# Performance work log

Hardware: AMD Instinct MI355X
Metric: run time of the kernel (lower is better)

Reference implementation:

```python
import jax, jax.numpy as jnp
import numpy as np

B, T, H = 32, 512, 1024
NT, NE = 8, 24          # padded per-sample trigger / entity span counts
C_TAGS = 50             # len(all_triggers_entities)
C = C_TAGS + 2          # + START/STOP for CRF
START, STOP = C_TAGS, C_TAGS + 1
A = 36                  # len(all_arguments)
D = 256                 # MLP hidden


def setup_inputs() -> dict:
    key = jax.random.key(0)
    ks = jax.random.split(key, 16)
    s = 0.02
    enc = jax.random.normal(ks[0], (B, T, H), jnp.float32)
    fc_W1 = jax.random.normal(ks[1], (H, D), jnp.float32) * s
    fc_b1 = jnp.zeros((D,), jnp.float32)
    fc_W2 = jax.random.normal(ks[2], (D, C), jnp.float32) * s
    fc_b2 = jnp.zeros((C,), jnp.float32)
    transitions = jax.random.normal(ks[3], (C, C), jnp.float32) * 0.01
    arg_W1 = jax.random.normal(ks[4], (2 * H, D), jnp.float32) * s
    arg_b1 = jnp.zeros((D,), jnp.float32)
    arg_W2 = jax.random.normal(ks[5], (D, A), jnp.float32) * s
    arg_b2 = jnp.zeros((A,), jnp.float32)
    tags = jax.random.randint(ks[6], (B, T), 0, C_TAGS)
    lengths = jax.random.randint(ks[7], (B,), T // 2, T + 1)
    trig_starts = jax.random.randint(ks[8], (B, NT), 0, T - 17)
    trig_ends = trig_starts + jax.random.randint(ks[9], (B, NT), 1, 17)
    trig_mask = (jnp.arange(NT)[None, :] < jax.random.randint(ks[10], (B, 1), 1, NT + 1)).astype(jnp.int32)
    ent_starts = jax.random.randint(ks[11], (B, NE), 0, T - 17)
    ent_ends = ent_starts + jax.random.randint(ks[12], (B, NE), 1, 17)
    ent_mask = (jnp.arange(NE)[None, :] < jax.random.randint(ks[13], (B, 1), 1, NE + 1)).astype(jnp.int32)
    return dict(encoder_out=enc, fc_W1=fc_W1, fc_b1=fc_b1, fc_W2=fc_W2, fc_b2=fc_b2,
                transitions=transitions, arg_W1=arg_W1, arg_b1=arg_b1, arg_W2=arg_W2, arg_b2=arg_b2,
                tags=tags, lengths=lengths,
                trig_starts=trig_starts, trig_ends=trig_ends, trig_mask=trig_mask,
                ent_starts=ent_starts, ent_ends=ent_ends, ent_mask=ent_mask)


def _crf_nll(feats, tags, mask, trans):
    # standard linear-chain CRF negative log likelihood, masked, summed over batch
    maskf = mask.astype(feats.dtype)
    alpha0 = feats[:, 0] + trans[START][None, :]            # [B,C]

    def step(alpha, xs):
        feat_t, m_t = xs                                    # [B,C], [B]
        new = jax.nn.logsumexp(alpha[:, :, None] + trans[None, :, :], axis=1) + feat_t
        return jnp.where(m_t[:, None] > 0, new, alpha), None

    alpha, _ = jax.lax.scan(step, alpha0,
                            (jnp.swapaxes(feats[:, 1:], 0, 1), jnp.swapaxes(mask[:, 1:], 0, 1)))
    logZ = jax.nn.logsumexp(alpha + trans[:, STOP][None, :], axis=1)  # [B]

    emit = jnp.take_along_axis(feats, tags[:, :, None], axis=2)[:, :, 0]
    emit_score = jnp.sum(emit * maskf, axis=1)
    trans_score = jnp.sum(trans[tags[:, :-1], tags[:, 1:]] * maskf[:, 1:], axis=1)
    start_score = trans[START, tags[:, 0]]
    last_idx = jnp.sum(mask, axis=1).astype(jnp.int32) - 1
    last_tag = jnp.take_along_axis(tags, last_idx[:, None], axis=1)[:, 0]
    stop_score = trans[last_tag, STOP]
    gold = emit_score + trans_score + start_score + stop_score
    return jnp.sum(logZ - gold)


def _span_mean(cs, starts, ends):
    # cs: exclusive prefix sums [B,T+1,H]; mean of encoder_out[i, s:e] per span
    s = jnp.take_along_axis(cs, starts[:, :, None], axis=1)
    e = jnp.take_along_axis(cs, ends[:, :, None], axis=1)
    return (e - s) / (ends - starts)[:, :, None].astype(cs.dtype)


def reference(encoder_out, fc_W1, fc_b1, fc_W2, fc_b2, transitions,
              arg_W1, arg_b1, arg_W2, arg_b2,
              tags, lengths, trig_starts, trig_ends, trig_mask,
              ent_starts, ent_ends, ent_mask):
    mask = (jnp.arange(T)[None, :] < lengths[:, None]).astype(jnp.int32)
    # trigger head: Linear -> Dropout(eval=identity) -> Linear (no activation, as in the source)
    feats = (encoder_out @ fc_W1 + fc_b1) @ fc_W2 + fc_b2   # [B,T,C]
    trigger_loss = _crf_nll(feats, tags, mask, transitions)

    # ragged span mean-pooling via prefix sums (replaces the per-sample python loop)
    cs = jnp.concatenate([jnp.zeros((B, 1, H), encoder_out.dtype),
                          jnp.cumsum(encoder_out, axis=1)], axis=1)  # [B,T+1,H]
    trig_vec = _span_mean(cs, trig_starts, trig_ends)       # [B,NT,H]
    ent_vec = _span_mean(cs, ent_starts, ent_ends)          # [B,NE,H]

    # cross product of (trigger, entity) per sample; concat order [entity, trigger]
    ent_b = jnp.broadcast_to(ent_vec[:, None, :, :], (B, NT, NE, H))
    trig_b = jnp.broadcast_to(trig_vec[:, :, None, :], (B, NT, NE, H))
    hidden = jnp.concatenate([ent_b, trig_b], axis=-1).reshape(B * NT * NE, 2 * H)
    logits = (hidden @ arg_W1 + arg_b1) @ arg_W2 + arg_b2   # [B*NT*NE, A]
    pair_mask = (trig_mask[:, :, None] * ent_mask[:, None, :]).reshape(-1).astype(logits.dtype)
    logits = logits * pair_mask[:, None]
    return trigger_loss, logits
```

## Files before the change

kernel.cpp:

```cpp
#include <hip/hip_runtime.h>
#include <math.h>

#define BB 32
#define TT 512
#define HH 1024
#define DD 256
#define CC 52
#define NTT 8
#define NEE 24
#define AA 36
#define STARTT 50
#define STOPP 51
#define NCH 16
#define CL 32

static const size_t OFF_WAT    = 0;
static const size_t OFF_BA     = 73728;
static const size_t OFF_ESTART = 73792;
static const size_t OFF_ESTOP  = 73856;
static const size_t OFF_BEFF   = 73920;
static const size_t OFF_EA     = 73984;
static const size_t OFF_WPACK  = 76032;
static const size_t OFF_FEATS  = 108800;
static const size_t OFF_EF64   = 960768;
static const size_t OFF_RMAT   = 2009344;
static const size_t OFF_TVEC   = 4106496;
static const size_t OFF_EVEC   = 4368640;
static const size_t OFF_TLOG   = 5155072;
static const size_t OFF_ELOG   = 5164288;
static const size_t OFF_LOSS   = 5191936;
static const size_t OFF_RED    = 5191968;

typedef __bf16 bf16x8 __attribute__((ext_vector_type(8)));
typedef float f32x4 __attribute__((ext_vector_type(4)));
typedef unsigned int uint4v __attribute__((ext_vector_type(4)));

union U4B { uint4v u; bf16x8 b; };

typedef const __attribute__((address_space(1))) void gvoid_t;
typedef __attribute__((address_space(3))) void lvoid_t;
#define GLOAD16(g, l) __builtin_amdgcn_global_load_lds((gvoid_t*)(g), (lvoid_t*)(l), 16, 0, 0)

static __device__ __forceinline__ unsigned int rne_bf16(float x) {
    unsigned int u = __float_as_uint(x);
    u += 0x7FFFu + ((u >> 16) & 1u);
    return u >> 16;
}

__global__ __launch_bounds__(256) void k1_prep_span(
    const float* __restrict__ enc,
    const float* __restrict__ fc_W1, const float* __restrict__ fc_b1,
    const float* __restrict__ fc_W2, const float* __restrict__ fc_b2,
    const float* __restrict__ trans,
    const float* __restrict__ arg_W1, const float* __restrict__ arg_b1,
    const float* __restrict__ arg_W2, const float* __restrict__ arg_b2,
    const int* __restrict__ ts, const int* __restrict__ te,
    const int* __restrict__ es, const int* __restrict__ ee,
    float* __restrict__ ws)
{
    int bid = blockIdx.x, tid = threadIdx.x;
    if (bid < 128) {
        int g = bid * 256 + tid;
        int s = g >> 2, i = g & 3;
        int kb = s >> 8, nb = (s >> 6) & 3, ln = s & 63;
        int c16 = ln & 15, hi = ln >> 4;
        int n = nb * 16 + c16;
        int k0 = kb * 32 + 8 * hi + 2 * i;
        unsigned int val = 0;
        if (n < CC) {
            const float* w1a = fc_W1 + (size_t)k0 * DD;
            const float* w1b = w1a + DD;
            float a0 = 0.f, a1 = 0.f;
            for (int d = 0; d < DD; ++d) {
                float w2 = fc_W2[d * CC + n];
                a0 = fmaf(w1a[d], w2, a0);
                a1 = fmaf(w1b[d], w2, a1);
            }
            val = rne_bf16(a0) | (rne_bf16(a1) << 16);
        }
        ((unsigned int*)(ws + OFF_WPACK))[g] = val;
    } else if (bid < 416) {
        int f = (bid - 128) * 256 + tid;
        int h = f / 36, a = f - h * 36;
        const float* w1 = arg_W1 + (size_t)h * DD;
        const float* w2 = arg_W2 + a;
        float a0 = 0.f, a1 = 0.f, a2 = 0.f, a3 = 0.f;
        for (int d = 0; d < DD; d += 4) {
            float4 w = *(const float4*)&w1[d];
            a0 = fmaf(w.x, w2[(size_t)(d + 0) * AA], a0);
            a1 = fmaf(w.y, w2[(size_t)(d + 1) * AA], a1);
            a2 = fmaf(w.z, w2[(size_t)(d + 2) * AA], a2);
            a3 = fmaf(w.w, w2[(size_t)(d + 3) * AA], a3);
        }
        ws[OFF_WAT + f] = (a0 + a1) + (a2 + a3);
    } else if (bid < 1440) {
        int sid = bid - 416;
        int b = sid >> 5, s = sid & 31;
        int st, en; float* outv;
        if (s < NTT) {
            st = ts[b * NTT + s]; en = te[b * NTT + s];
            outv = ws + OFF_TVEC + ((size_t)b * NTT + s) * HH;
        } else {
            int e = s - NTT;
            st = es[b * NEE + e]; en = ee[b * NEE + e];
            outv = ws + OFF_EVEC + ((size_t)b * NEE + e) * HH;
        }
        int h4 = tid * 4;
        float ax = 0, ay = 0, az = 0, aw = 0;
        for (int t = st; t < en; ++t) {
            float4 v = *(const float4*)&enc[((size_t)b * TT + t) * HH + h4];
            ax += v.x; ay += v.y; az += v.z; aw += v.w;
        }
        float inv = 1.f / (float)(en - st);
        float4 o; o.x = ax * inv; o.y = ay * inv; o.z = az * inv; o.w = aw * inv;
        *(float4*)&outv[h4] = o;
    } else {
        int f = (bid - 1440) * 256 + tid;
        if (f < 2048) {
            int m = f >> 5, kp = f & 31;
            int k0 = 2 * kp;
            unsigned int wlo = 0, whi = 0;
            if (m < 52) {
                if (k0 < 52)     wlo = rne_bf16(expf(trans[k0 * CC + m]) * 0.015625f);
                if (k0 + 1 < 52) whi = rne_bf16(expf(trans[(k0 + 1) * CC + m]) * 0.015625f);
            }
            ((unsigned int*)(ws + OFF_EA))[f] = wlo | (whi << 16);
        } else if (f < 2112) {
            int j = f - 2048;
            ws[OFF_ESTART + j] = (j < 52) ? expf(trans[STARTT * CC + j]) : 0.f;
        } else if (f < 2176) {
            int j = f - 2112;
            ws[OFF_ESTOP + j] = (j < 52) ? expf(trans[j * CC + STOPP]) : 0.f;
        } else if (f < 2240) {
            int c = f - 2176;
            float acc = 0.f;
            if (c < 52) {
                acc = fc_b2[c];
                for (int d = 0; d < DD; ++d) acc = fmaf(fc_b1[d], fc_W2[d * CC + c], acc);
            }
            ws[OFF_BEFF + c] = acc;
        } else if (f < 2304) {
            int a = f - 2240;
            float acc = 0.f;
            if (a < 36) {
                acc = arg_b2[a];
                for (int d = 0; d < DD; ++d) acc = fmaf(arg_b1[d], arg_W2[d * AA + a], acc);
            }
            ws[OFF_BA + a] = acc;
        } else if (f < 2306) {
            ((unsigned*)(ws + OFF_RED))[f - 2304] = 0u;
        }
    }
}

__global__ __launch_bounds__(256) void k2_feats_arg(
    const float* __restrict__ enc, float* __restrict__ ws)
{
    __shared__ f32x4 Ab[2][1024];
    __shared__ uint4v Bb[2][512];
    int bid = blockIdx.x, tid = threadIdx.x;
    int wid = tid >> 6, lane = tid & 63;

    if (bid >= 256) {
        int id = (bid - 256) * 4 + wid;
        int b = id >> 5, s = id & 31;
        int a = lane;
        const float* vec; const float* wt; float* outv; float base;
        if (s < NTT) {
            vec = ws + OFF_TVEC + ((size_t)b * NTT + s) * HH;
            wt  = ws + OFF_WAT + (size_t)1024 * AA;
            outv = ws + OFF_TLOG + ((size_t)b * NTT + s) * AA;
            base = (a < AA) ? ws[OFF_BA + a] : 0.f;
        } else {
            int e = s - NTT;
            vec = ws + OFF_EVEC + ((size_t)b * NEE + e) * HH;
            wt  = ws + OFF_WAT;
            outv = ws + OFF_ELOG + ((size_t)b * NEE + e) * AA;
            base = 0.f;
        }
        if (a < AA) {
            float a0 = 0, a1 = 0, a2 = 0, a3 = 0;
            for (int h = 0; h < HH; h += 4) {
                float4 vv = *(const float4*)&vec[h];
                a0 = fmaf(vv.x, wt[(size_t)(h + 0) * AA + a], a0);
                a1 = fmaf(vv.y, wt[(size_t)(h + 1) * AA + a], a1);
                a2 = fmaf(vv.z, wt[(size_t)(h + 2) * AA + a], a2);
                a3 = fmaf(vv.w, wt[(size_t)(h + 3) * AA + a], a3);
            }
            outv[a] = base + ((a0 + a1) + (a2 + a3));
        }
        return;
    }

    const uint4v* Wpack = (const uint4v*)(ws + OFF_WPACK);
    float* feats = ws + OFF_FEATS;
    float* ef64  = ws + OFF_EF64;
    int c16 = lane & 15, hi = lane >> 4;
    int c7 = c16 & 7;
    int row0 = bid * 64;
    int rowW = wid * 16 + c16;

    f32x4 acc[4];
#pragma unroll
    for (int nb = 0; nb < 4; ++nb) {
        float bv = ws[OFF_BEFF + nb * 16 + c16];
        acc[nb][0] = bv; acc[nb][1] = bv; acc[nb][2] = bv; acc[nb][3] = bv;
    }
    {
#pragma unroll
        for (int i = 0; i < 4; ++i) {
            int f = i * 256 + tid;
            int row = f >> 4, qp = f & 15;
            int q = (qp & 8) | ((qp & 7) ^ (row & 7));
            GLOAD16(enc + (size_t)(row0 + row) * HH + q * 4, &Ab[0][i * 256 + wid * 64]);
        }
#pragma unroll
        for (int i = 0; i < 2; ++i) {
            GLOAD16(Wpack + i * 256 + tid, &Bb[0][i * 256 + wid * 64]);
        }
    }
    for (int it = 0; it < 16; ++it) {
        __syncthreads();
        if (it < 15) {
            int buf = (it + 1) & 1;
            int k0 = (it + 1) * 64;
#pragma unroll
            for (int i = 0; i < 4; ++i) {
                int f = i * 256 + tid;
                int row = f >> 4, qp = f & 15;
                int q = (qp & 8) | ((qp & 7) ^ (row & 7));
                GLOAD16(enc + (size_t)(row0 + row) * HH + k0 + q * 4, &Ab[buf][i * 256 + wid * 64]);
            }
#pragma unroll
            for (int i = 0; i < 2; ++i) {
                GLOAD16(Wpack + (size_t)(it + 1) * 512 + i * 256 + tid, &Bb[buf][i * 256 + wid * 64]);
            }
        }
        int cb = it & 1;
#pragma unroll
        for (int kbL = 0; kbL < 2; ++kbL) {
            int q0 = (kbL * 8) | ((2 * hi) ^ c7);
            int q1 = q0 ^ 1;
            f32x4 a0 = Ab[cb][rowW * 16 + q0];
            f32x4 a1 = Ab[cb][rowW * 16 + q1];
            f32x4 lo = (c7 & 1) ? a1 : a0;
            f32x4 hf = (c7 & 1) ? a0 : a1;
            unsigned u0, u1, u2, u3;
            asm("v_cvt_pk_bf16_f32 %0, %1, %2" : "=v"(u0) : "v"(lo[0]), "v"(lo[1]));
            asm("v_cvt_pk_bf16_f32 %0, %1, %2" : "=v"(u1) : "v"(lo[2]), "v"(lo[3]));
            asm("v_cvt_pk_bf16_f32 %0, %1, %2" : "=v"(u2) : "v"(hf[0]), "v"(hf[1]));
            asm("v_cvt_pk_bf16_f32 %0, %1, %2" : "=v"(u3) : "v"(hf[2]), "v"(hf[3]));
            U4B A; A.u[0] = u0; A.u[1] = u1; A.u[2] = u2; A.u[3] = u3;
#pragma unroll
            for (int nb = 0; nb < 4; ++nb) {
                U4B Bf; Bf.u = Bb[cb][kbL * 256 + nb * 64 + lane];
                acc[nb] = __builtin_amdgcn_mfma_f32_16x16x32_bf16(A.b, Bf.b, acc[nb], 0, 0, 0);
            }
        }
    }
#pragma unroll
    for (int nb = 0; nb < 4; ++nb) {
        int col = nb * 16 + c16;
#pragma unroll
        for (int r = 0; r < 4; ++r) {
            size_t grow = row0 + wid * 16 + hi * 4 + r;
            float v = acc[nb][r];
            if (col < CC) {
                feats[grow * CC + col] = v;
                ef64[grow * 64 + col] = expf(v);
            } else {
                ef64[grow * 64 + col] = 0.f;
            }
        }
    }
}

__global__ __launch_bounds__(64) void k3_chunk(
    const int* __restrict__ lengths, float* __restrict__ ws)
{
    int bid = blockIdx.x;
    int lane = threadIdx.x;

    const unsigned short* EA = (const unsigned short*)(ws + OFF_EA);
    const float* ef64 = ws + OFF_EF64;
    unsigned int* Rout = (unsigned int*)(ws + OFF_RMAT);
    int b = bid >> 6;
    int ch = (bid >> 2) & (NCH - 1);
    int nb = bid & 3;
    int c16 = lane & 15, hi = lane >> 4;
    int len = lengths[b];
    int t0 = 1 + ch * CL;
    int Le = len - t0; if (Le > CL) Le = CL;
    unsigned int* outm = Rout + (((size_t)b * NCH + ch) << 11);

    if (Le <= 0) {
#pragma unroll
        for (int q = 0; q < 8; ++q) {
            int col0 = nb * 16 + 2 * q;
            unsigned int val = 0;
            if (lane < 52) {
                if (col0 == lane)          val = 0x3F80u;
                else if (col0 + 1 == lane) val = 0x3F800000u;
            }
            outm[lane * 32 + nb * 8 + q] = val;
        }
        return;
    }

    bf16x8 Afr[4][2];
#pragma unroll
    for (int mb = 0; mb < 4; ++mb)
#pragma unroll
        for (int kb = 0; kb < 2; ++kb) {
            U4B x; x.u = *(const uint4v*)(EA + (size_t)(mb * 16 + c16) * 64 + kb * 32 + 8 * hi);
            Afr[mb][kb] = x.b;
        }

    unsigned int Bw[2][4];
#pragma unroll
    for (int kb = 0; kb < 2; ++kb)
#pragma unroll
        for (int j = 0; j < 4; ++j) {
            int col = nb * 16 + c16;
            int k0 = kb * 32 + 8 * hi + 2 * j;
            unsigned int v = 0;
            if (col < 52) {
                if (k0 == col)          v = 0x3F80u;
                else if (k0 + 1 == col) v = 0x3F800000u;
            }
            Bw[kb][j] = v;
        }

    unsigned int W[4][2];
    int hsel = hi >> 1;
    int src0 = c16 + 32 * (hi & 1);
    int src1 = src0 + 16;
    const float* efb = ef64 + (size_t)b * TT * 64;

    for (int s = 0; s < Le; ++s) {
        int t = t0 + s;
        U4B b0; b0.u = uint4v{Bw[0][0], Bw[0][1], Bw[0][2], Bw[0][3]};
        U4B b1; b1.u = uint4v{Bw[1][0], Bw[1][1], Bw[1][2], Bw[1][3]};
        f32x4 D[4];
#pragma unroll
        for (int mb = 0; mb < 4; ++mb) {
            f32x4 z = {0.f, 0.f, 0.f, 0.f};
            z = __builtin_amdgcn_mfma_f32_16x16x32_bf16(Afr[mb][0], b0.b, z, 0, 0, 0);
            z = __builtin_amdgcn_mfma_f32_16x16x32_bf16(Afr[mb][1], b1.b, z, 0, 0, 0);
            D[mb] = z;
        }
#pragma unroll
        for (int mb = 0; mb < 4; ++mb) {
            f32x4 cv = *(const f32x4*)(efb + (size_t)t * 64 + mb * 16 + 4 * hi);
            float d0 = D[mb][0] * cv[0];
            float d1 = D[mb][1] * cv[1];
            float d2 = D[mb][2] * cv[2];
            float d3 = D[mb][3] * cv[3];
            unsigned int w0, w1;
            asm("v_cvt_pk_bf16_f32 %0, %1, %2" : "=v"(w0) : "v"(d0), "v"(d1));
            asm("v_cvt_pk_bf16_f32 %0, %1, %2" : "=v"(w1) : "v"(d2), "v"(d3));
            W[mb][0] = w0; W[mb][1] = w1;
        }
#pragma unroll
        for (int kb = 0; kb < 2; ++kb)
#pragma unroll
            for (int j = 0; j < 4; ++j) {
                int src = (j < 2) ? src0 : src1;
                unsigned int va = (unsigned int)__shfl((int)W[2 * kb][j & 1], src, 64);
                unsigned int vb = (unsigned int)__shfl((int)W[2 * kb + 1][j & 1], src, 64);
                Bw[kb][j] = hsel ? vb : va;
            }
    }

#pragma unroll
    for (int mb = 0; mb < 4; ++mb)
#pragma unroll
        for (int w = 0; w < 2; ++w) {
            unsigned int my = W[mb][w];
            unsigned int ot = (unsigned int)__shfl_xor((int)my, 1, 64);
            unsigned int val;
            int r = 16 * mb + 4 * hi + 2 * w + (c16 & 1);
            if ((c16 & 1) == 0) val = (my & 0xFFFFu) | (ot << 16);
            else                val = (ot >> 16) | (my & 0xFFFF0000u);
            outm[r * 32 + nb * 8 + (c16 >> 1)] = val;
        }
}

__global__ __launch_bounds__(256) void k4_final(
    const float* __restrict__ trans,
    const int* __restrict__ tags, const int* __restrict__ lengths,
    const int* __restrict__ tmask, const int* __restrict__ emask,
    float* __restrict__ ws, float* __restrict__ out)
{
    __shared__ float vsh[64];
    int bid = blockIdx.x, tid = threadIdx.x;
    if (bid >= 32) {
        int idx = (bid - 32) * 256 + tid;
        int a = idx % AA;
        int p = idx / AA;
        int ne = p % NEE;
        int q = p / NEE;
        int nt = q & 7;
        int b = q >> 3;
        float m = (float)(tmask[b * NTT + nt] * emask[b * NEE + ne]);
        out[1 + idx] = (ws[OFF_TLOG + ((size_t)b * NTT + nt) * AA + a] +
                        ws[OFF_ELOG + ((size_t)b * NEE + ne) * AA + a]) * m;
        return;
    }
    if (tid >= 64) return;
    int b = bid, lane = tid;
    int len = lengths[b];
    const unsigned int* Rb = (const unsigned int*)(ws + OFF_RMAT) + ((size_t)b << 15);
    float v = 0.f;
    if (lane < 52) v = ws[OFF_ESTART + lane] * ws[OFF_EF64 + (size_t)b * TT * 64 + lane];
    int S = 0;

    uint4v bf0[8], bf1[8], bf2[8];

#define LOADM(BUF, IDX)                                                        \
    {                                                                          \
        const unsigned int* rr = Rb + (size_t)(IDX) * 2048 + (size_t)lane * 32;\
        _Pragma("unroll")                                                      \
        for (int q = 0; q < 8; ++q) BUF[q] = *(const uint4v*)(rr + q * 4);     \
    }

#define MATVEC(BUF)                                                            \
    {                                                                          \
        vsh[lane] = v;                                                         \
        float c0 = 0, c1 = 0, c2 = 0, c3 = 0;                                  \
        _Pragma("unroll")                                                      \
        for (int q = 0; q < 8; ++q) {                                          \
            uint4v u = BUF[q];                                                 \
            float4 va = *(const float4*)&vsh[q * 8];                           \
            float4 vb = *(const float4*)&vsh[q * 8 + 4];                       \
            c0 = fmaf(__uint_as_float(u[0] << 16), va.x, c0);                  \
            c0 = fmaf(__uint_as_float(u[0] & 0xFFFF0000u), va.y, c0);          \
            c1 = fmaf(__uint_as_float(u[1] << 16), va.z, c1);                  \
            c1 = fmaf(__uint_as_float(u[1] & 0xFFFF0000u), va.w, c1);          \
            c2 = fmaf(__uint_as_float(u[2] << 16), vb.x, c2);                  \
            c2 = fmaf(__uint_as_float(u[2] & 0xFFFF0000u), vb.y, c2);          \
            c3 = fmaf(__uint_as_float(u[3] << 16), vb.z, c3);                  \
            c3 = fmaf(__uint_as_float(u[3] & 0xFFFF0000u), vb.w, c3);          \
        }                                                                      \
        float acc = (c0 + c1) + (c2 + c3);                                     \
        float M = acc;                                                         \
        _Pragma("unroll")                                                      \
        for (int o = 32; o >= 1; o >>= 1) M = fmaxf(M, __shfl_xor(M, o, 64));  \
        int e = (int)((__float_as_uint(M) >> 23) & 0xFF) - 127;                \
        acc *= __uint_as_float((unsigned)(127 - e) << 23);                     \
        S += e; v = acc;                                                       \
    }

    LOADM(bf0, 0) LOADM(bf1, 1)
    LOADM(bf2,  2) MATVEC(bf0)
    LOADM(bf0,  3) MATVEC(bf1)
    LOADM(bf1,  4) MATVEC(bf2)
    LOADM(bf2,  5) MATVEC(bf0)
    LOADM(bf0,  6) MATVEC(bf1)
    LOADM(bf1,  7) MATVEC(bf2)
    LOADM(bf2,  8) MATVEC(bf0)
    LOADM(bf0,  9) MATVEC(bf1)
    LOADM(bf1, 10) MATVEC(bf2)
    LOADM(bf2, 11) MATVEC(bf0)
    LOADM(bf0, 12) MATVEC(bf1)
    LOADM(bf1, 13) MATVEC(bf2)
    LOADM(bf2, 14) MATVEC(bf0)
    LOADM(bf0, 15) MATVEC(bf1)
    MATVEC(bf2)
    MATVEC(bf0)
#undef LOADM
#undef MATVEC

    float z = (lane < 52) ? v * ws[OFF_ESTOP + lane] : 0.f;
#pragma unroll
    for (int o = 32; o >= 1; o >>= 1) z += __shfl_xor(z, o, 64);
    float logZ = logf(z) + (float)(S + 6 * (len - 1)) * 0.6931471805599453f;

    const int* tg = tags + (size_t)b * TT;
    const float* fb = ws + OFF_FEATS + (size_t)b * TT * CC;
    float g = 0.f;
    for (int t = lane; t < TT; t += 64) {
        if (t < len) {
            int ct = tg[t];
            g += fb[(size_t)t * CC + ct];
            if (t + 1 < len) g += trans[ct * CC + tg[t + 1]];
        }
    }
#pragma unroll
    for (int o = 32; o >= 1; o >>= 1) g += __shfl_xor(g, o, 64);

    unsigned old = 0;
    if (lane == 0) {
        g += trans[STARTT * CC + tg[0]] + trans[tg[len - 1] * CC + STOPP];
        ws[OFF_LOSS + b] = logZ - g;
        __threadfence();
        unsigned* lcnt = (unsigned*)(ws + OFF_RED);
        old = __hip_atomic_fetch_add(lcnt, 1u, __ATOMIC_ACQ_REL, __HIP_MEMORY_SCOPE_AGENT);
    }
    old = (unsigned)__shfl((int)old, 0, 64);
    if (old == BB - 1) {
        __threadfence();
        float tv = (lane < BB) ? ((volatile float*)(ws + OFF_LOSS))[lane] : 0.f;
#pragma unroll
        for (int o = 32; o >= 1; o >>= 1) tv += __shfl_xor(tv, o, 64);
        if (lane == 0) out[0] = tv;
    }
}

extern "C" void kernel_launch(void* const* d_in, const int* in_sizes, int n_in,
                              void* d_out, int out_size, void* d_ws, size_t ws_size,
                              hipStream_t stream)
{
    const float* enc    = (const float*)d_in[0];
    const float* fc_W1  = (const float*)d_in[1];
    const float* fc_b1  = (const float*)d_in[2];
    const float* fc_W2  = (const float*)d_in[3];
    const float* fc_b2  = (const float*)d_in[4];
    const float* trans  = (const float*)d_in[5];
    const float* arg_W1 = (const float*)d_in[6];
    const float* arg_b1 = (const float*)d_in[7];
    const float* arg_W2 = (const float*)d_in[8];
    const float* arg_b2 = (const float*)d_in[9];
    const int* tags     = (const int*)d_in[10];
    const int* lengths  = (const int*)d_in[11];
    const int* tstarts  = (const int*)d_in[12];
    const int* tends    = (const int*)d_in[13];
    const int* tmask    = (const int*)d_in[14];
    const int* estarts  = (const int*)d_in[15];
    const int* eends    = (const int*)d_in[16];
    const int* emask    = (const int*)d_in[17];
    float* out = (float*)d_out;
    float* ws  = (float*)d_ws;

    hipLaunchKernelGGL(k1_prep_span, dim3(1450), dim3(256), 0, stream,
                       enc, fc_W1, fc_b1, fc_W2, fc_b2, trans,
                       arg_W1, arg_b1, arg_W2, arg_b2,
                       tstarts, tends, estarts, eends, ws);
    hipLaunchKernelGGL(k2_feats_arg, dim3(512), dim3(256), 0, stream,
                       enc, ws);
    hipLaunchKernelGGL(k3_chunk, dim3(2048), dim3(64), 0, stream,
                       lengths, ws);
    hipLaunchKernelGGL(k4_final, dim3(896), dim3(256), 0, stream,
                       trans, tags, lengths, tmask, emask, ws, out);
}
```

Baseline: 102.9 us.

## Move arg-logit blocks into chunk kernel, pack chunk waves, deepen matrix prefetch

The per-span argument-logit matvec blocks move out of the feats GEMM kernel and into the CRF chunk kernel, so the GEMM launches only its 256 MFMA tiles. The chunk kernel now packs four 64-lane chunk tasks per 256-thread block (512 blocks) and appends the arg-logit blocks after them, for 768 blocks in total. Separately, the final CRF chain matvec now cycles through four register buffers instead of three, keeping more matrix loads in flight at the cost of extra registers. The aim is to balance load across kernels, cut block count, and hide more global-load latency in the serial chain, with some risk to occupancy.

Result: faster. 100.0 us (-2.8%).

```diff
diff --git a/kernel.cpp b/kernel.cpp
--- a/kernel.cpp
+++ b/kernel.cpp
@@ -153,7 +153,7 @@
     }
 }
 
-__global__ __launch_bounds__(256) void k2_feats_arg(
+__global__ __launch_bounds__(256) void k2_feats(
     const float* __restrict__ enc, float* __restrict__ ws)
 {
     __shared__ f32x4 Ab[2][1024];
@@ -161,8 +161,97 @@
     int bid = blockIdx.x, tid = threadIdx.x;
     int wid = tid >> 6, lane = tid & 63;
 
-    if (bid >= 256) {
-        int id = (bid - 256) * 4 + wid;
+    const uint4v* Wpack = (const uint4v*)(ws + OFF_WPACK);
+    float* feats = ws + OFF_FEATS;
+    float* ef64  = ws + OFF_EF64;
+    int c16 = lane & 15, hi = lane >> 4;
+    int c7 = c16 & 7;
+    int row0 = bid * 64;
+    int rowW = wid * 16 + c16;
+
+    f32x4 acc[4];
+#pragma unroll
+    for (int nb = 0; nb < 4; ++nb) {
+        float bv = ws[OFF_BEFF + nb * 16 + c16];
+        acc[nb][0] = bv; acc[nb][1] = bv; acc[nb][2] = bv; acc[nb][3] = bv;
+    }
+    {
+#pragma unroll
+        for (int i = 0; i < 4; ++i) {
+            int f = i * 256 + tid;
+            int row = f >> 4, qp = f & 15;
+            int q = (qp & 8) | ((qp & 7) ^ (row & 7));
+            GLOAD16(enc + (size_t)(row0 + row) * HH + q * 4, &Ab[0][i * 256 + wid * 64]);
+        }
+#pragma unroll
+        for (int i = 0; i < 2; ++i) {
+            GLOAD16(Wpack + i * 256 + tid, &Bb[0][i * 256 + wid * 64]);
+        }
+    }
+    for (int it = 0; it < 16; ++it) {
+        __syncthreads();
+        if (it < 15) {
+            int buf = (it + 1) & 1;
+            int k0 = (it + 1) * 64;
+#pragma unroll
+            for (int i = 0; i < 4; ++i) {
+                int f = i * 256 + tid;
+                int row = f >> 4, qp = f & 15;
+                int q = (qp & 8) | ((qp & 7) ^ (row & 7));
+                GLOAD16(enc + (size_t)(row0 + row) * HH + k0 + q * 4, &Ab[buf][i * 256 + wid * 64]);
+            }
+#pragma unroll
+            for (int i = 0; i < 2; ++i) {
+                GLOAD16(Wpack + (size_t)(it + 1) * 512 + i * 256 + tid, &Bb[buf][i * 256 + wid * 64]);
+            }
+        }
+        int cb = it & 1;
+#pragma unroll
+        for (int kbL = 0; kbL < 2; ++kbL) {
+            int q0 = (kbL * 8) | ((2 * hi) ^ c7);
+            int q1 = q0 ^ 1;
+            f32x4 a0 = Ab[cb][rowW * 16 + q0];
+            f32x4 a1 = Ab[cb][rowW * 16 + q1];
+            f32x4 lo = (c7 & 1) ? a1 : a0;
+            f32x4 hf = (c7 & 1) ? a0 : a1;
+            unsigned u0, u1, u2, u3;
+            asm("v_cvt_pk_bf16_f32 %0, %1, %2" : "=v"(u0) : "v"(lo[0]), "v"(lo[1]));
+            asm("v_cvt_pk_bf16_f32 %0, %1, %2" : "=v"(u1) : "v"(lo[2]), "v"(lo[3]));
+            asm("v_cvt_pk_bf16_f32 %0, %1, %2" : "=v"(u2) : "v"(hf[0]), "v"(hf[1]));
+            asm("v_cvt_pk_bf16_f32 %0, %1, %2" : "=v"(u3) : "v"(hf[2]), "v"(hf[3]));
+            U4B A; A.u[0] = u0; A.u[1] = u1; A.u[2] = u2; A.u[3] = u3;
+#pragma unroll
+            for (int nb = 0; nb < 4; ++nb) {
+                U4B Bf; Bf.u = Bb[cb][kbL * 256 + nb * 64 + lane];
+                acc[nb] = __builtin_amdgcn_mfma_f32_16x16x32_bf16(A.b, Bf.b, acc[nb], 0, 0, 0);
+            }
+        }
+    }
+#pragma unroll
+    for (int nb = 0; nb < 4; ++nb) {
+        int col = nb * 16 + c16;
+#pragma unroll
+        for (int r = 0; r < 4; ++r) {
+            size_t grow = row0 + wid * 16 + hi * 4 + r;
+            float v = acc[nb][r];
+            if (col < CC) {
+                feats[grow * CC + col] = v;
+                ef64[grow * 64 + col] = expf(v);
+            } else {
+                ef64[grow * 64 + col] = 0.f;
+            }
+        }
+    }
+}
+
+__global__ __launch_bounds__(256) void k3_chunk_arg(
+    const int* __restrict__ lengths, float* __restrict__ ws)
+{
+    int bid = blockIdx.x, tid = threadIdx.x;
+    int wid = tid >> 6, lane = tid & 63;
+
+    if (bid >= 512) {
+        int id = (bid - 512) * 4 + wid;
         int b = id >> 5, s = id & 31;
         int a = lane;
         const float* vec; const float* wt; float* outv; float base;
@@ -192,101 +281,13 @@
         return;
     }
 
-    const uint4v* Wpack = (const uint4v*)(ws + OFF_WPACK);
-    float* feats = ws + OFF_FEATS;
-    float* ef64  = ws + OFF_EF64;
-    int c16 = lane & 15, hi = lane >> 4;
-    int c7 = c16 & 7;
-    int row0 = bid * 64;
-    int rowW = wid * 16 + c16;
-
-    f32x4 acc[4];
-#pragma unroll
-    for (int nb = 0; nb < 4; ++nb) {
-        float bv = ws[OFF_BEFF + nb * 16 + c16];
-        acc[nb][0] = bv; acc[nb][1] = bv; acc[nb][2] = bv; acc[nb][3] = bv;
-    }
-    {
-#pragma unroll
-        for (int i = 0; i < 4; ++i) {
-            int f = i * 256 + tid;
-            int row = f >> 4, qp = f & 15;
-            int q = (qp & 8) | ((qp & 7) ^ (row & 7));
-            GLOAD16(enc + (size_t)(row0 + row) * HH + q * 4, &Ab[0][i * 256 + wid * 64]);
-        }
-#pragma unroll
-        for (int i = 0; i < 2; ++i) {
-            GLOAD16(Wpack + i * 256 + tid, &Bb[0][i * 256 + wid * 64]);
-        }
-    }
-    for (int it = 0; it < 16; ++it) {
-        __syncthreads();
-        if (it < 15) {
-            int buf = (it + 1) & 1;
-            int k0 = (it + 1) * 64;
-#pragma unroll
-            for (int i = 0; i < 4; ++i) {
-                int f = i * 256 + tid;
-                int row = f >> 4, qp = f & 15;
-                int q = (qp & 8) | ((qp & 7) ^ (row & 7));
-                GLOAD16(enc + (size_t)(row0 + row) * HH + k0 + q * 4, &Ab[buf][i * 256 + wid * 64]);
-            }
-#pragma unroll
-            for (int i = 0; i < 2; ++i) {
-                GLOAD16(Wpack + (size_t)(it + 1) * 512 + i * 256 + tid, &Bb[buf][i * 256 + wid * 64]);
-            }
-        }
-        int cb = it & 1;
-#pragma unroll
-        for (int kbL = 0; kbL < 2; ++kbL) {
-            int q0 = (kbL * 8) | ((2 * hi) ^ c7);
-            int q1 = q0 ^ 1;
-            f32x4 a0 = Ab[cb][rowW * 16 + q0];
-            f32x4 a1 = Ab[cb][rowW * 16 + q1];
-            f32x4 lo = (c7 & 1) ? a1 : a0;
-            f32x4 hf = (c7 & 1) ? a0 : a1;
-            unsigned u0, u1, u2, u3;
-            asm("v_cvt_pk_bf16_f32 %0, %1, %2" : "=v"(u0) : "v"(lo[0]), "v"(lo[1]));
-            asm("v_cvt_pk_bf16_f32 %0, %1, %2" : "=v"(u1) : "v"(lo[2]), "v"(lo[3]));
-            asm("v_cvt_pk_bf16_f32 %0, %1, %2" : "=v"(u2) : "v"(hf[0]), "v"(hf[1]));
-            asm("v_cvt_pk_bf16_f32 %0, %1, %2" : "=v"(u3) : "v"(hf[2]), "v"(hf[3]));
-            U4B A; A.u[0] = u0; A.u[1] = u1; A.u[2] = u2; A.u[3] = u3;
-#pragma unroll
-            for (int nb = 0; nb < 4; ++nb) {
-                U4B Bf; Bf.u = Bb[cb][kbL * 256 + nb * 64 + lane];
-                acc[nb] = __builtin_amdgcn_mfma_f32_16x16x32_bf16(A.b, Bf.b, acc[nb], 0, 0, 0);
-            }
-        }
-    }
-#pragma unroll
-    for (int nb = 0; nb < 4; ++nb) {
-        int col = nb * 16 + c16;
-#pragma unroll
-        for (int r = 0; r < 4; ++r) {
-            size_t grow = row0 + wid * 16 + hi * 4 + r;
-            float v = acc[nb][r];
-            if (col < CC) {
-                feats[grow * CC + col] = v;
-                ef64[grow * 64 + col] = expf(v);
-            } else {
-                ef64[grow * 64 + col] = 0.f;
-            }
-        }
-    }
-}
-
-__global__ __launch_bounds__(64) void k3_chunk(
-    const int* __restrict__ lengths, float* __restrict__ ws)
-{
-    int bid = blockIdx.x;
-    int lane = threadIdx.x;
-
+    int cuid = bid * 4 + wid;
     const unsigned short* EA = (const unsigned short*)(ws + OFF_EA);
     const float* ef64 = ws + OFF_EF64;
     unsigned int* Rout = (unsigned int*)(ws + OFF_RMAT);
-    int b = bid >> 6;
-    int ch = (bid >> 2) & (NCH - 1);
-    int nb = bid & 3;
+    int b = cuid >> 6;
+    int ch = (cuid >> 2) & (NCH - 1);
+    int nb = cuid & 3;
     int c16 = lane & 15, hi = lane >> 4;
     int len = lengths[b];
     int t0 = 1 + ch * CL;
@@ -415,7 +416,7 @@
     if (lane < 52) v = ws[OFF_ESTART + lane] * ws[OFF_EF64 + (size_t)b * TT * 64 + lane];
     int S = 0;
 
-    uint4v bf0[8], bf1[8], bf2[8];
+    uint4v bf0[8], bf1[8], bf2[8], bf3[8];
 
 #define LOADM(BUF, IDX)                                                        \
     {                                                                          \
@@ -451,23 +452,23 @@
         S += e; v = acc;                                                       \
     }
 
-    LOADM(bf0, 0) LOADM(bf1, 1)
-    LOADM(bf2,  2) MATVEC(bf0)
-    LOADM(bf0,  3) MATVEC(bf1)
-    LOADM(bf1,  4) MATVEC(bf2)
-    LOADM(bf2,  5) MATVEC(bf0)
-    LOADM(bf0,  6) MATVEC(bf1)
-    LOADM(bf1,  7) MATVEC(bf2)
-    LOADM(bf2,  8) MATVEC(bf0)
-    LOADM(bf0,  9) MATVEC(bf1)
-    LOADM(bf1, 10) MATVEC(bf2)
-    LOADM(bf2, 11) MATVEC(bf0)
+    LOADM(bf0, 0) LOADM(bf1, 1) LOADM(bf2, 2) LOADM(bf3, 3)
+    MATVEC(bf0)
+    LOADM(bf0,  4) MATVEC(bf1)
+    LOADM(bf1,  5) MATVEC(bf2)
+    LOADM(bf2,  6) MATVEC(bf3)
+    LOADM(bf3,  7) MATVEC(bf0)
+    LOADM(bf0,  8) MATVEC(bf1)
+    LOADM(bf1,  9) MATVEC(bf2)
+    LOADM(bf2, 10) MATVEC(bf3)
+    LOADM(bf3, 11) MATVEC(bf0)
     LOADM(bf0, 12) MATVEC(bf1)
     LOADM(bf1, 13) MATVEC(bf2)
-    LOADM(bf2, 14) MATVEC(bf0)
-    LOADM(bf0, 15) MATVEC(bf1)
+    LOADM(bf2, 14) MATVEC(bf3)
+    LOADM(bf3, 15) MATVEC(bf0)
+    MATVEC(bf1)
     MATVEC(bf2)
-    MATVEC(bf0)
+    MATVEC(bf3)
 #undef LOADM
 #undef MATVEC
 
@@ -536,9 +537,9 @@
                        enc, fc_W1, fc_b1, fc_W2, fc_b2, trans,
                        arg_W1, arg_b1, arg_W2, arg_b2,
                        tstarts, tends, estarts, eends, ws);
-    hipLaunchKernelGGL(k2_feats_arg, dim3(512), dim3(256), 0, stream,
+    hipLaunchKernelGGL(k2_feats, dim3(256), dim3(256), 0, stream,
                        enc, ws);
-    hipLaunchKernelGGL(k3_chunk, dim3(2048), dim3(64), 0, stream,
+    hipLaunchKernelGGL(k3_chunk_arg, dim3(768), dim3(256), 0, stream,
                        lengths, ws);
     hipLaunchKernelGGL(k4_final, dim3(896), dim3(256), 0, stream,
                        trans, tags, lengths, tmask, emask, ws, out);
```
